# Performance work log

Measured on AMD Instinct MI355X. Metric: run time of the kernel, lower is better.

The kernel has to match this reference:

```python
import jax, jax.numpy as jnp
import numpy as np

K = 3          # cfg.KNN_UP
CHUNK = 2048   # point chunk for brute-force KNN
BN_EPS = 1e-5


def knn_interp(vox_c, vox_f, pt_c):
    """Inverse-distance k-NN interpolation of voxel features onto points.
    vox_c: [Nv,3] voxel centers; vox_f: [Nv,C]; pt_c: [Np,3]. Returns [Np,C]."""
    Np = pt_c.shape[0]

    def chunk_fn(pc):  # pc: [CHUNK,3]
        d2 = jnp.sum((pc[:, None, :] - vox_c[None, :, :]) ** 2, axis=-1)  # [CHUNK,Nv]
        neg_d2, idx = jax.lax.top_k(-d2, K)                               # k nearest
        d = jnp.sqrt(jnp.maximum(-neg_d2, 0.0))
        w = 1.0 / (d + 1e-8)
        w = w / jnp.sum(w, axis=-1, keepdims=True)                        # [CHUNK,K]
        return jnp.sum(vox_f[idx] * w[..., None], axis=1)                 # [CHUNK,C]

    out = jax.lax.map(chunk_fn, pt_c.reshape(Np // CHUNK, CHUNK, 3))
    return out.reshape(Np, vox_f.shape[-1])


def bn1d(x, gamma, beta):
    # BatchNorm1d in training mode, applied per decomposed batch item (as in
    # the original per-sample list comprehension): stats over the point dim.
    mu = jnp.mean(x, axis=0, keepdims=True)
    var = jnp.var(x, axis=0, keepdims=True)
    return gamma * (x - mu) * jax.lax.rsqrt(var + BN_EPS) + beta


def level_forward(vox_c, vox_f, pt_c, gamma, beta):
    f = jax.vmap(knn_interp, in_axes=(0, 0, 0))(vox_c, vox_f, pt_c)  # [B,Np,C]
    return jax.vmap(lambda xf: bn1d(xf, gamma, beta))(f)


def setup_inputs() -> dict:
    key = jax.random.key(0)
    ks = jax.random.split(key, 16)
    B, Np = 2, 32768
    SCENE = 50.0  # spread coordinates over a ~50m scene
    nvs = [2048, 6144, 16384, 32768]
    chs = [256, 128, 96, 96]
    inp = {"pt_c": jax.random.uniform(ks[0], (B, Np, 3), jnp.float32) * SCENE}
    for i, (nv, c) in enumerate(zip(nvs, chs), start=1):
        inp[f"vox_c{i}"] = jax.random.uniform(ks[2 * i - 1], (B, nv, 3), jnp.float32) * SCENE
        inp[f"vox_f{i}"] = jax.random.normal(ks[2 * i], (B, nv, c), jnp.float32)
        inp[f"gamma{i}"] = jnp.ones((c,), jnp.float32)
        inp[f"beta{i}"] = jnp.zeros((c,), jnp.float32)
    return inp


def reference(pt_c, vox_c1, vox_f1, gamma1, beta1,
              vox_c2, vox_f2, gamma2, beta2,
              vox_c3, vox_f3, gamma3, beta3,
              vox_c4, vox_f4, gamma4, beta4):
    # voxel_to_point: per-level KNN upsampling of decoder voxel features to
    # the raw point cloud, followed by per-sample BatchNorm1d.
    f1 = level_forward(vox_c1, vox_f1, pt_c, gamma1, beta1)
    f2 = level_forward(vox_c2, vox_f2, pt_c, gamma2, beta2)
    f3 = level_forward(vox_c3, vox_f3, pt_c, gamma3, beta3)
    f4 = level_forward(vox_c4, vox_f4, pt_c, gamma4, beta4)
    return (f1, f2, f3, f4)
```

## Files before the change

kernel.cpp:

```cpp
#include <hip/hip_runtime.h>
#include <cfloat>
#include <climits>
#include <cstdint>

#define NPOINTS 32768
#define NBATCH  2
#define NLEV    4
#define NJOB    5
#define PG      16
#define PCELLS  (PG*PG*PG)
#define NPB     128
#define NBLK    (NPOINTS / NPB)

struct BinJob {
  const float* coords;
  int* cnt; int* start; int* cur;
  float4* sorted;
  int G, ncells, N;
  float invh;
};
struct BinParams { BinJob job[NJOB]; };

struct Level {
  const float4* sorted;
  const int*    start;
  int*          idxo;
  float*        wo;
  int G, ncells, Nv;
  float h, invh;
};
struct Params { Level lv[NLEV]; };

__device__ __forceinline__ int cell1d(float x, float invh, int G) {
  int c = (int)(x * invh);
  return min(max(c, 0), G - 1);
}

__global__ __launch_bounds__(256) void zero_kernel(int* __restrict__ p, int n)
{
  int i = blockIdx.x * 256 + threadIdx.x;
  if (i < n) p[i] = 0;
}

__global__ __launch_bounds__(256) void count_kernel(BinParams prm)
{
  const BinJob J = prm.job[blockIdx.z];
  int v = blockIdx.x * 256 + threadIdx.x;
  int b = blockIdx.y;
  if (v >= J.N) return;
  const float* p = J.coords + ((size_t)b * J.N + v) * 3;
  int cx = cell1d(p[0], J.invh, J.G), cy = cell1d(p[1], J.invh, J.G), cz = cell1d(p[2], J.invh, J.G);
  atomicAdd(&J.cnt[b * J.ncells + (cz * J.G + cy) * J.G + cx], 1);
}

__global__ __launch_bounds__(1024) void scan_kernel(BinParams prm)
{
  const BinJob J = prm.job[blockIdx.y];
  const int b = blockIdx.x, t = threadIdx.x;
  const int ncells = J.ncells;
  const int* c  = J.cnt + (size_t)b * ncells;
  int* st = J.start + (size_t)b * (ncells + 1);
  int* cu = J.cur + (size_t)b * ncells;
  __shared__ int part[1024];
  const int chunk = (ncells + 1023) / 1024;
  const int lo = t * chunk, hi = min(lo + chunk, ncells);
  int s = 0;
  for (int i = lo; i < hi; ++i) s += c[i];
  part[t] = s;
  __syncthreads();
  for (int off = 1; off < 1024; off <<= 1) {
    int v = (t >= off) ? part[t - off] : 0;
    __syncthreads();
    part[t] += v;
    __syncthreads();
  }
  int base = (t > 0) ? part[t - 1] : 0;
  for (int i = lo; i < hi; ++i) { st[i] = base; cu[i] = base; base += c[i]; }
  if (t == 1023) st[ncells] = part[1023];
}

__global__ __launch_bounds__(256) void scatter_kernel(BinParams prm)
{
  const BinJob J = prm.job[blockIdx.z];
  int v = blockIdx.x * 256 + threadIdx.x;
  int b = blockIdx.y;
  if (v >= J.N) return;
  const float* p = J.coords + ((size_t)b * J.N + v) * 3;
  float x = p[0], y = p[1], z = p[2];
  int cx = cell1d(x, J.invh, J.G), cy = cell1d(y, J.invh, J.G), cz = cell1d(z, J.invh, J.G);
  int pos = atomicAdd(&J.cur[b * J.ncells + (cz * J.G + cy) * J.G + cx], 1);
  J.sorted[(size_t)b * J.N + pos] = make_float4(x, y, z, __int_as_float(v));
}

__global__ __launch_bounds__(256) void query_kernel(
    const float4* __restrict__ psorted, Params prm)
{
  const int l = blockIdx.y, b = blockIdx.z;
  const Level L = prm.lv[l];
  const int tid = threadIdx.x;
  const int q = tid & 3;
  const int sp = blockIdx.x * 64 + (tid >> 2);
  float4 pt = psorted[(size_t)b * NPOINTS + sp];
  const float px = pt.x, py = pt.y, pz = pt.z;
  const int p = __float_as_int(pt.w);
  const int G = L.G;
  const float h = L.h;

  const int cx = cell1d(px, L.invh, G);
  const int cy = cell1d(py, L.invh, G);
  const int cz = cell1d(pz, L.invh, G);
  const float fx = px - cx * h, fy = py - cy * h, fz = pz - cz * h;
  float m = fminf(fminf(fminf(fx, h - fx), fminf(fy, h - fy)), fminf(fz, h - fz));
  m = fmaxf(m, 0.f);

  const int* start     = L.start  + (size_t)b * (L.ncells + 1);
  const float4* sorted = L.sorted + (size_t)b * L.Nv;

  float b0 = FLT_MAX, b1 = FLT_MAX, b2 = FLT_MAX;
  int   i0 = INT_MAX, i1 = INT_MAX, i2 = INT_MAX;

  auto ins = [&](float d2, int vi) {
    if (d2 < b2 || (d2 == b2 && vi < i2)) {
      if (d2 < b1 || (d2 == b1 && vi < i1)) {
        b2 = b1; i2 = i1;
        if (d2 < b0 || (d2 == b0 && vi < i0)) { b1 = b0; i1 = i0; b0 = d2; i0 = vi; }
        else                                  { b1 = d2; i1 = vi; }
      } else { b2 = d2; i2 = vi; }
    }
  };
  auto cand = [&](int k) {
    float4 vv = sorted[k];
    int vi = __float_as_int(vv.w);
    float dx = px - vv.x, dy = py - vv.y, dz = pz - vv.z;
    float d2 = __fadd_rn(__fadd_rn(__fmul_rn(dx, dx), __fmul_rn(dy, dy)),
                         __fmul_rn(dz, dz));
    ins(d2, vi);
  };
  auto scan_range = [&](int ks, int ke) {
    for (int k = ks + q; k < ke; k += 4) cand(k);
  };

  const int rmax = max(max(cx, G - 1 - cx), max(max(cy, G - 1 - cy), max(cz, G - 1 - cz)));
  for (int rho = 0; rho <= rmax; ++rho) {
    if (rho >= 1) {
      float bm = fminf(b2, __shfl_xor(b2, 1));
      bm = fminf(bm, __shfl_xor(bm, 2));
      float dmin = fmaxf((rho - 1) * h + m, 0.f);
      if (dmin * dmin * 0.99999f > bm) break;
    }
    const int z0 = max(cz - rho, 0), z1 = min(cz + rho, G - 1);
    const int y0 = max(cy - rho, 0), y1 = min(cy + rho, G - 1);
    for (int iz = z0; iz <= z1; ++iz) {
      const int adz = abs(iz - cz);
      for (int iy = y0; iy <= y1; ++iy) {
        const int ady = max(adz, abs(iy - cy));
        const int row = (iz * G + iy) * G;
        if (ady == rho) {
          const int x0 = max(cx - rho, 0), x1 = min(cx + rho, G - 1);
          scan_range(start[row + x0], start[row + x1 + 1]);
        } else {
          const int xl = cx - rho, xr = cx + rho;
          if (xl >= 0)     scan_range(start[row + xl], start[row + xl + 1]);
          if (xr <= G - 1) scan_range(start[row + xr], start[row + xr + 1]);
        }
      }
    }
  }

  #pragma unroll
  for (int mask = 1; mask <= 2; mask <<= 1) {
    float c0 = __shfl_xor(b0, mask), c1 = __shfl_xor(b1, mask), c2 = __shfl_xor(b2, mask);
    int   j0 = __shfl_xor(i0, mask), j1 = __shfl_xor(i1, mask), j2 = __shfl_xor(i2, mask);
    ins(c0, j0); ins(c1, j1); ins(c2, j2);
  }

  if (q == 0) {
    float w0 = 1.0f / (sqrtf(b0) + 1e-8f);
    float w1 = 1.0f / (sqrtf(b1) + 1e-8f);
    float w2 = 1.0f / (sqrtf(b2) + 1e-8f);
    float ws = (w0 + w1) + w2;
    size_t o = ((size_t)b * NPOINTS + p) * 3;
    L.idxo[o] = i0; L.idxo[o + 1] = i1; L.idxo[o + 2] = i2;
    L.wo[o] = w0 / ws; L.wo[o + 1] = w1 / ws; L.wo[o + 2] = w2 / ws;
  }
}

template <int C, int BDIM>
__global__ __launch_bounds__(BDIM) void interp_kernel(
    const float* __restrict__ voxf, const int* __restrict__ idxo,
    const float* __restrict__ wo, float* __restrict__ out,
    float* __restrict__ psum, float* __restrict__ psq, int Nv)
{
  constexpr int C4 = C / 4;
  constexpr int R  = BDIM / C4;
  const int b = blockIdx.y, blk = blockIdx.x;
  const int tid = threadIdx.x;
  const int r = tid / C4, c4 = tid - r * C4;
  const float4* fb = (const float4*)(voxf + (size_t)b * Nv * C);
  float4* ob = (float4*)(out + (size_t)b * NPOINTS * C);
  const int p0 = blk * NPB;

  float4 s = make_float4(0, 0, 0, 0), q = make_float4(0, 0, 0, 0);
  for (int p = p0 + r; p < p0 + NPB; p += R) {
    size_t pg = ((size_t)b * NPOINTS + p) * 3;
    int   ia = idxo[pg], ib = idxo[pg + 1], ic = idxo[pg + 2];
    float wa = wo[pg],   wb = wo[pg + 1],   wc = wo[pg + 2];
    float4 fa = fb[(size_t)ia * C4 + c4];
    float4 f2 = fb[(size_t)ib * C4 + c4];
    float4 fc = fb[(size_t)ic * C4 + c4];
    float4 o;
    o.x = wa * fa.x + wb * f2.x + wc * fc.x;
    o.y = wa * fa.y + wb * f2.y + wc * fc.y;
    o.z = wa * fa.z + wb * f2.z + wc * fc.z;
    o.w = wa * fa.w + wb * f2.w + wc * fc.w;
    ob[(size_t)p * C4 + c4] = o;
    s.x += o.x; s.y += o.y; s.z += o.z; s.w += o.w;
    q.x += o.x * o.x; q.y += o.y * o.y; q.z += o.z * o.z; q.w += o.w * o.w;
  }

  __shared__ float4 ls[BDIM];
  ls[tid] = s;
  __syncthreads();
  if (r == 0) {
    float4 tot = s;
    #pragma unroll
    for (int rr = 1; rr < R; ++rr) {
      float4 v = ls[c4 + rr * C4];
      tot.x += v.x; tot.y += v.y; tot.z += v.z; tot.w += v.w;
    }
    ((float4*)psum)[((size_t)b * NBLK + blk) * C4 + c4] = tot;
  }
  __syncthreads();
  ls[tid] = q;
  __syncthreads();
  if (r == 0) {
    float4 tot = q;
    #pragma unroll
    for (int rr = 1; rr < R; ++rr) {
      float4 v = ls[c4 + rr * C4];
      tot.x += v.x; tot.y += v.y; tot.z += v.z; tot.w += v.w;
    }
    ((float4*)psq)[((size_t)b * NBLK + blk) * C4 + c4] = tot;
  }
}

__global__ __launch_bounds__(256) void bn_stats_kernel(
    const float* __restrict__ psum, const float* __restrict__ psq,
    const float* __restrict__ gamma, const float* __restrict__ beta,
    float* __restrict__ scale, float* __restrict__ shift, int C, float invN)
{
  const int c = blockIdx.x, b = blockIdx.y, t = threadIdx.x;
  float s = 0.f, q = 0.f;
  for (int k = t; k < NBLK; k += 256) {
    s += psum[((size_t)b * NBLK + k) * C + c];
    q += psq[((size_t)b * NBLK + k) * C + c];
  }
  __shared__ float ss[256], qs[256];
  ss[t] = s; qs[t] = q;
  __syncthreads();
  for (int o = 128; o > 0; o >>= 1) {
    if (t < o) { ss[t] += ss[t + o]; qs[t] += qs[t + o]; }
    __syncthreads();
  }
  if (t == 0) {
    float mu  = ss[0] * invN;
    float var = fmaxf(qs[0] * invN - mu * mu, 0.f);
    float sc  = gamma[c] * rsqrtf(var + 1e-5f);
    scale[b * C + c] = sc;
    shift[b * C + c] = beta[c] - mu * sc;
  }
}

__global__ __launch_bounds__(256) void bn_apply_kernel(
    float* __restrict__ out, const float* __restrict__ scale,
    const float* __restrict__ shift, int C, int NpC)
{
  const int e = blockIdx.x * 256 + threadIdx.x;
  const int npc4 = NpC >> 2, c4n = C >> 2;
  const int b = e / npc4;
  const int rem = e - b * npc4;
  const int c4 = rem % c4n;
  float4 v  = ((float4*)out)[e];
  float4 sc = ((const float4*)scale)[b * c4n + c4];
  float4 sh = ((const float4*)shift)[b * c4n + c4];
  v.x = fmaf(v.x, sc.x, sh.x);
  v.y = fmaf(v.y, sc.y, sh.y);
  v.z = fmaf(v.z, sc.z, sh.z);
  v.w = fmaf(v.w, sc.w, sh.w);
  ((float4*)out)[e] = v;
}

extern "C" void kernel_launch(void* const* d_in, const int* in_sizes, int n_in,
                              void* d_out, int out_size, void* d_ws, size_t ws_size,
                              hipStream_t stream)
{
  const float* ptc = (const float*)d_in[0];
  static const int    Cs[4]     = {256, 128, 96, 96};
  static const int    Nvs[4]    = {2048, 6144, 16384, 32768};
  static const int    Gs[4]     = {10, 14, 18, 22};
  static const size_t outOff[4] = {0, 16777216, 25165824, 31457280};

  size_t off = 0;
  auto carve = [&](size_t bytes) {
    off = (off + 255) & ~(size_t)255;
    size_t o = off; off += bytes; return o;
  };
  char* w = (char*)d_ws;

  int nc[NJOB];
  for (int l = 0; l < 4; ++l) nc[l] = Gs[l] * Gs[l] * Gs[l];
  nc[4] = PCELLS;
  int Ns[NJOB] = {Nvs[0], Nvs[1], Nvs[2], Nvs[3], NPOINTS};
  int Gj[NJOB] = {Gs[0], Gs[1], Gs[2], Gs[3], PG};

  int totcnt = 0;
  for (int j = 0; j < NJOB; ++j) totcnt += nc[j];
  int* cntbase = (int*)(w + carve((size_t)NBATCH * totcnt * 4));

  float4* sortedj[NJOB]; int* cntj[NJOB]; int* sttj[NJOB]; int* curj[NJOB];
  {
    int acc = 0;
    for (int j = 0; j < NJOB; ++j) {
      cntj[j] = cntbase + (size_t)NBATCH * acc;
      acc += nc[j];
    }
  }
  for (int j = 0; j < NJOB; ++j) {
    sortedj[j] = (float4*)(w + carve((size_t)NBATCH * Ns[j] * 16));
    sttj[j]    = (int*)   (w + carve((size_t)NBATCH * (nc[j] + 1) * 4));
    curj[j]    = (int*)   (w + carve((size_t)NBATCH * nc[j] * 4));
  }
  int*   idxo  = (int*)  (w + carve((size_t)NLEV * NBATCH * NPOINTS * 3 * 4));
  float* wo    = (float*)(w + carve((size_t)NLEV * NBATCH * NPOINTS * 3 * 4));
  float* psum  = (float*)(w + carve((size_t)NBATCH * NBLK * 256 * 4));
  float* psq   = (float*)(w + carve((size_t)NBATCH * NBLK * 256 * 4));
  float* scale = (float*)(w + carve((size_t)NBATCH * 256 * 4));
  float* shift = (float*)(w + carve((size_t)NBATCH * 256 * 4));

  BinParams bp;
  for (int j = 0; j < NJOB; ++j) {
    BinJob& J = bp.job[j];
    J.coords = (j < 4) ? (const float*)d_in[1 + 4 * j] : ptc;
    J.cnt = cntj[j]; J.start = sttj[j]; J.cur = curj[j]; J.sorted = sortedj[j];
    J.G = Gj[j]; J.ncells = nc[j]; J.N = Ns[j];
    J.invh = Gj[j] / 50.0f;
  }

  Params prm;
  for (int l = 0; l < 4; ++l) {
    Level& L = prm.lv[l];
    L.sorted = sortedj[l]; L.start = sttj[l];
    L.idxo = idxo + (size_t)l * NBATCH * NPOINTS * 3;
    L.wo   = wo   + (size_t)l * NBATCH * NPOINTS * 3;
    L.G = Gs[l]; L.ncells = nc[l]; L.Nv = Nvs[l];
    L.h = 50.0f / Gs[l]; L.invh = Gs[l] / 50.0f;
  }

  const int zn = NBATCH * totcnt;
  zero_kernel<<<(zn + 255) / 256, 256, 0, stream>>>(cntbase, zn);
  count_kernel<<<dim3((NPOINTS + 255) / 256, NBATCH, NJOB), 256, 0, stream>>>(bp);
  scan_kernel<<<dim3(NBATCH, NJOB), 1024, 0, stream>>>(bp);
  scatter_kernel<<<dim3((NPOINTS + 255) / 256, NBATCH, NJOB), 256, 0, stream>>>(bp);

  query_kernel<<<dim3(NPOINTS / 64, NLEV, NBATCH), 256, 0, stream>>>(sortedj[4], prm);

  for (int l = 0; l < 4; ++l) {
    const float* voxf  = (const float*)d_in[2 + 4 * l];
    const float* gamma = (const float*)d_in[3 + 4 * l];
    const float* beta  = (const float*)d_in[4 + 4 * l];
    const int C = Cs[l], Nv = Nvs[l];
    float* outl = (float*)d_out + outOff[l];
    const int* idl = idxo + (size_t)l * NBATCH * NPOINTS * 3;
    const float* wl = wo  + (size_t)l * NBATCH * NPOINTS * 3;

    if (C == 256)
      interp_kernel<256, 256><<<dim3(NBLK, NBATCH), 256, 0, stream>>>(
          voxf, idl, wl, outl, psum, psq, Nv);
    else if (C == 128)
      interp_kernel<128, 256><<<dim3(NBLK, NBATCH), 256, 0, stream>>>(
          voxf, idl, wl, outl, psum, psq, Nv);
    else
      interp_kernel<96, 240><<<dim3(NBLK, NBATCH), 240, 0, stream>>>(
          voxf, idl, wl, outl, psum, psq, Nv);

    bn_stats_kernel<<<dim3(C, NBATCH), 256, 0, stream>>>(
        psum, psq, gamma, beta, scale, shift, C, 1.0f / NPOINTS);

    const int n4 = NBATCH * NPOINTS * C / 4;
    bn_apply_kernel<<<n4 / 256, 256, 0, stream>>>(
        (float*)outl, scale, shift, C, NPOINTS * C);
  }
}
```

Baseline: 338.9 us.

## Recompute interpolation in BN apply pass and finer voxel grids with cell-level work split

Interpolation now runs twice: a first pass computes only the BN partial statistics without writing output, and a second pass recomputes the weighted gather, applies scale/shift and writes to the original point index. This removes the intermediate output write plus the separate read-modify-write BN apply pass. The query kernel stores results in sorted-point order, distributes whole cells round-robin across the four lanes instead of striding within cells, and uses finer grids. A per-cell insertion sort of points by original index is added to keep the ordering deterministic. The cost is recomputing the gathers and possible load imbalance across lanes.

```diff
diff --git a/kernel.cpp b/kernel.cpp
--- a/kernel.cpp
+++ b/kernel.cpp
@@ -92,6 +92,23 @@
   J.sorted[(size_t)b * J.N + pos] = make_float4(x, y, z, __int_as_float(v));
 }
 
+__global__ __launch_bounds__(256) void cellsort_kernel(
+    float4* __restrict__ sorted, const int* __restrict__ start)
+{
+  int cid = blockIdx.x * 256 + threadIdx.x;
+  if (cid >= NBATCH * PCELLS) return;
+  int b = cid / PCELLS, cc = cid - b * PCELLS;
+  const int* st = start + (size_t)b * (PCELLS + 1);
+  float4* s = sorted + (size_t)b * NPOINTS;
+  int ks = st[cc], ke = st[cc + 1];
+  for (int i = ks + 1; i < ke; ++i) {
+    float4 v = s[i]; int key = __float_as_int(v.w);
+    int j = i - 1;
+    while (j >= ks && __float_as_int(s[j].w) > key) { s[j + 1] = s[j]; --j; }
+    s[j + 1] = v;
+  }
+}
+
 __global__ __launch_bounds__(256) void query_kernel(
     const float4* __restrict__ psorted, Params prm)
 {
@@ -102,7 +119,6 @@
   const int sp = blockIdx.x * 64 + (tid >> 2);
   float4 pt = psorted[(size_t)b * NPOINTS + sp];
   const float px = pt.x, py = pt.y, pz = pt.z;
-  const int p = __float_as_int(pt.w);
   const int G = L.G;
   const float h = L.h;
 
@@ -128,19 +144,19 @@
       } else { b2 = d2; i2 = vi; }
     }
   };
-  auto cand = [&](int k) {
-    float4 vv = sorted[k];
-    int vi = __float_as_int(vv.w);
-    float dx = px - vv.x, dy = py - vv.y, dz = pz - vv.z;
-    float d2 = __fadd_rn(__fadd_rn(__fmul_rn(dx, dx), __fmul_rn(dy, dy)),
-                         __fmul_rn(dz, dz));
-    ins(d2, vi);
+  auto scan_all = [&](int ks, int ke) {
+    for (int k = ks; k < ke; ++k) {
+      float4 vv = sorted[k];
+      int vi = __float_as_int(vv.w);
+      float dx = px - vv.x, dy = py - vv.y, dz = pz - vv.z;
+      float d2 = __fadd_rn(__fadd_rn(__fmul_rn(dx, dx), __fmul_rn(dy, dy)),
+                           __fmul_rn(dz, dz));
+      ins(d2, vi);
+    }
   };
-  auto scan_range = [&](int ks, int ke) {
-    for (int k = ks + q; k < ke; k += 4) cand(k);
-  };
 
   const int rmax = max(max(cx, G - 1 - cx), max(max(cy, G - 1 - cy), max(cz, G - 1 - cz)));
+  int task = 0;
   for (int rho = 0; rho <= rmax; ++rho) {
     if (rho >= 1) {
       float bm = fminf(b2, __shfl_xor(b2, 1));
@@ -157,11 +173,11 @@
         const int row = (iz * G + iy) * G;
         if (ady == rho) {
           const int x0 = max(cx - rho, 0), x1 = min(cx + rho, G - 1);
-          scan_range(start[row + x0], start[row + x1 + 1]);
+          if (((task++) & 3) == q) scan_all(start[row + x0], start[row + x1 + 1]);
         } else {
           const int xl = cx - rho, xr = cx + rho;
-          if (xl >= 0)     scan_range(start[row + xl], start[row + xl + 1]);
-          if (xr <= G - 1) scan_range(start[row + xr], start[row + xr + 1]);
+          if (xl >= 0)     { if (((task++) & 3) == q) scan_all(start[row + xl], start[row + xl + 1]); }
+          if (xr <= G - 1) { if (((task++) & 3) == q) scan_all(start[row + xr], start[row + xr + 1]); }
         }
       }
     }
@@ -179,16 +195,16 @@
     float w1 = 1.0f / (sqrtf(b1) + 1e-8f);
     float w2 = 1.0f / (sqrtf(b2) + 1e-8f);
     float ws = (w0 + w1) + w2;
-    size_t o = ((size_t)b * NPOINTS + p) * 3;
+    size_t o = ((size_t)b * NPOINTS + sp) * 3;
     L.idxo[o] = i0; L.idxo[o + 1] = i1; L.idxo[o + 2] = i2;
     L.wo[o] = w0 / ws; L.wo[o + 1] = w1 / ws; L.wo[o + 2] = w2 / ws;
   }
 }
 
 template <int C, int BDIM>
-__global__ __launch_bounds__(BDIM) void interp_kernel(
+__global__ __launch_bounds__(BDIM) void interp_stats_kernel(
     const float* __restrict__ voxf, const int* __restrict__ idxo,
-    const float* __restrict__ wo, float* __restrict__ out,
+    const float* __restrict__ wo,
     float* __restrict__ psum, float* __restrict__ psq, int Nv)
 {
   constexpr int C4 = C / 4;
@@ -197,12 +213,11 @@
   const int tid = threadIdx.x;
   const int r = tid / C4, c4 = tid - r * C4;
   const float4* fb = (const float4*)(voxf + (size_t)b * Nv * C);
-  float4* ob = (float4*)(out + (size_t)b * NPOINTS * C);
   const int p0 = blk * NPB;
 
   float4 s = make_float4(0, 0, 0, 0), q = make_float4(0, 0, 0, 0);
-  for (int p = p0 + r; p < p0 + NPB; p += R) {
-    size_t pg = ((size_t)b * NPOINTS + p) * 3;
+  for (int sp = p0 + r; sp < p0 + NPB; sp += R) {
+    size_t pg = ((size_t)b * NPOINTS + sp) * 3;
     int   ia = idxo[pg], ib = idxo[pg + 1], ic = idxo[pg + 2];
     float wa = wo[pg],   wb = wo[pg + 1],   wc = wo[pg + 2];
     float4 fa = fb[(size_t)ia * C4 + c4];
@@ -213,7 +228,6 @@
     o.y = wa * fa.y + wb * f2.y + wc * fc.y;
     o.z = wa * fa.z + wb * f2.z + wc * fc.z;
     o.w = wa * fa.w + wb * f2.w + wc * fc.w;
-    ob[(size_t)p * C4 + c4] = o;
     s.x += o.x; s.y += o.y; s.z += o.z; s.w += o.w;
     q.x += o.x * o.x; q.y += o.y * o.y; q.z += o.z * o.z; q.w += o.w * o.w;
   }
@@ -271,23 +285,39 @@
   }
 }
 
-__global__ __launch_bounds__(256) void bn_apply_kernel(
-    float* __restrict__ out, const float* __restrict__ scale,
-    const float* __restrict__ shift, int C, int NpC)
-{
-  const int e = blockIdx.x * 256 + threadIdx.x;
-  const int npc4 = NpC >> 2, c4n = C >> 2;
-  const int b = e / npc4;
-  const int rem = e - b * npc4;
-  const int c4 = rem % c4n;
-  float4 v  = ((float4*)out)[e];
-  float4 sc = ((const float4*)scale)[b * c4n + c4];
-  float4 sh = ((const float4*)shift)[b * c4n + c4];
-  v.x = fmaf(v.x, sc.x, sh.x);
-  v.y = fmaf(v.y, sc.y, sh.y);
-  v.z = fmaf(v.z, sc.z, sh.z);
-  v.w = fmaf(v.w, sc.w, sh.w);
-  ((float4*)out)[e] = v;
+template <int C, int BDIM>
+__global__ __launch_bounds__(BDIM) void interp_apply_kernel(
+    const float* __restrict__ voxf, const int* __restrict__ idxo,
+    const float* __restrict__ wo, const float4* __restrict__ psorted,
+    const float* __restrict__ scale, const float* __restrict__ shift,
+    float* __restrict__ out, int Nv)
+{
+  constexpr int C4 = C / 4;
+  constexpr int R  = BDIM / C4;
+  const int b = blockIdx.y, blk = blockIdx.x;
+  const int tid = threadIdx.x;
+  const int r = tid / C4, c4 = tid - r * C4;
+  const float4* fb = (const float4*)(voxf + (size_t)b * Nv * C);
+  float4* ob = (float4*)(out + (size_t)b * NPOINTS * C);
+  const float4 sc = ((const float4*)scale)[b * C4 + c4];
+  const float4 sh = ((const float4*)shift)[b * C4 + c4];
+  const int p0 = blk * NPB;
+
+  for (int sp = p0 + r; sp < p0 + NPB; sp += R) {
+    int p = __float_as_int(psorted[(size_t)b * NPOINTS + sp].w);
+    size_t pg = ((size_t)b * NPOINTS + sp) * 3;
+    int   ia = idxo[pg], ib = idxo[pg + 1], ic = idxo[pg + 2];
+    float wa = wo[pg],   wb = wo[pg + 1],   wc = wo[pg + 2];
+    float4 fa = fb[(size_t)ia * C4 + c4];
+    float4 f2 = fb[(size_t)ib * C4 + c4];
+    float4 fc = fb[(size_t)ic * C4 + c4];
+    float4 o;
+    o.x = fmaf(wa * fa.x + wb * f2.x + wc * fc.x, sc.x, sh.x);
+    o.y = fmaf(wa * fa.y + wb * f2.y + wc * fc.y, sc.y, sh.y);
+    o.z = fmaf(wa * fa.z + wb * f2.z + wc * fc.z, sc.z, sh.z);
+    o.w = fmaf(wa * fa.w + wb * f2.w + wc * fc.w, sc.w, sh.w);
+    ob[(size_t)p * C4 + c4] = o;
+  }
 }
 
 extern "C" void kernel_launch(void* const* d_in, const int* in_sizes, int n_in,
@@ -297,7 +327,7 @@
   const float* ptc = (const float*)d_in[0];
   static const int    Cs[4]     = {256, 128, 96, 96};
   static const int    Nvs[4]    = {2048, 6144, 16384, 32768};
-  static const int    Gs[4]     = {10, 14, 18, 22};
+  static const int    Gs[4]     = {13, 18, 25, 32};
   static const size_t outOff[4] = {0, 16777216, 25165824, 31457280};
 
   size_t off = 0;
@@ -361,6 +391,7 @@
   count_kernel<<<dim3((NPOINTS + 255) / 256, NBATCH, NJOB), 256, 0, stream>>>(bp);
   scan_kernel<<<dim3(NBATCH, NJOB), 1024, 0, stream>>>(bp);
   scatter_kernel<<<dim3((NPOINTS + 255) / 256, NBATCH, NJOB), 256, 0, stream>>>(bp);
+  cellsort_kernel<<<(NBATCH * PCELLS + 255) / 256, 256, 0, stream>>>(sortedj[4], sttj[4]);
 
   query_kernel<<<dim3(NPOINTS / 64, NLEV, NBATCH), 256, 0, stream>>>(sortedj[4], prm);
 
@@ -374,20 +405,26 @@
     const float* wl = wo  + (size_t)l * NBATCH * NPOINTS * 3;
 
     if (C == 256)
-      interp_kernel<256, 256><<<dim3(NBLK, NBATCH), 256, 0, stream>>>(
-          voxf, idl, wl, outl, psum, psq, Nv);
+      interp_stats_kernel<256, 256><<<dim3(NBLK, NBATCH), 256, 0, stream>>>(
+          voxf, idl, wl, psum, psq, Nv);
     else if (C == 128)
-      interp_kernel<128, 256><<<dim3(NBLK, NBATCH), 256, 0, stream>>>(
-          voxf, idl, wl, outl, psum, psq, Nv);
+      interp_stats_kernel<128, 256><<<dim3(NBLK, NBATCH), 256, 0, stream>>>(
+          voxf, idl, wl, psum, psq, Nv);
     else
-      interp_kernel<96, 240><<<dim3(NBLK, NBATCH), 240, 0, stream>>>(
-          voxf, idl, wl, outl, psum, psq, Nv);
+      interp_stats_kernel<96, 240><<<dim3(NBLK, NBATCH), 240, 0, stream>>>(
+          voxf, idl, wl, psum, psq, Nv);
 
     bn_stats_kernel<<<dim3(C, NBATCH), 256, 0, stream>>>(
         psum, psq, gamma, beta, scale, shift, C, 1.0f / NPOINTS);
 
-    const int n4 = NBATCH * NPOINTS * C / 4;
-    bn_apply_kernel<<<n4 / 256, 256, 0, stream>>>(
-        (float*)outl, scale, shift, C, NPOINTS * C);
-  }
-}
+    if (C == 256)
+      interp_apply_kernel<256, 256><<<dim3(NBLK, NBATCH), 256, 0, stream>>>(
+          voxf, idl, wl, sortedj[4], scale, shift, outl, Nv);
+    else if (C == 128)
+      interp_apply_kernel<128, 256><<<dim3(NBLK, NBATCH), 256, 0, stream>>>(
+          voxf, idl, wl, sortedj[4], scale, shift, outl, Nv);
+    else
+      interp_apply_kernel<96, 240><<<dim3(NBLK, NBATCH), 240, 0, stream>>>(
+          voxf, idl, wl, sortedj[4], scale, shift, outl, Nv);
+  }
+}
```

New measurement: 577.9 us. +70.5%, slower.

## Unroll first KNN shell, store results in sorted order, sort cells deterministically

Applied to the files above, without the earlier changes.

The query kernel now loads the 9 row ranges of the 3x3x3 neighbourhood up front and scans them without per-shell checks, falling back to the shell loop only when needed. It also writes idx/weight outputs in spatially sorted point order instead of scattering by original index. The interp kernel then maps each sorted slot back to its original point through the sorted point array. A new cellsort kernel insertion-sorts each point cell by index so the sorted order is deterministic despite the atomic scatter. The aim is fewer dependent start[] loads and coalesced query writes and interp reads, at the cost of an extra kernel and an extra indirection load in interp.

```diff
diff --git a/kernel.cpp b/kernel.cpp
--- a/kernel.cpp
+++ b/kernel.cpp
@@ -92,6 +92,23 @@
   J.sorted[(size_t)b * J.N + pos] = make_float4(x, y, z, __int_as_float(v));
 }
 
+__global__ __launch_bounds__(256) void cellsort_kernel(
+    float4* __restrict__ sorted, const int* __restrict__ start)
+{
+  int cid = blockIdx.x * 256 + threadIdx.x;
+  if (cid >= NBATCH * PCELLS) return;
+  int b = cid / PCELLS, cc = cid - b * PCELLS;
+  const int* st = start + (size_t)b * (PCELLS + 1);
+  float4* s = sorted + (size_t)b * NPOINTS;
+  int ks = st[cc], ke = st[cc + 1];
+  for (int i = ks + 1; i < ke; ++i) {
+    float4 v = s[i]; int key = __float_as_int(v.w);
+    int j = i - 1;
+    while (j >= ks && __float_as_int(s[j].w) > key) { s[j + 1] = s[j]; --j; }
+    s[j + 1] = v;
+  }
+}
+
 __global__ __launch_bounds__(256) void query_kernel(
     const float4* __restrict__ psorted, Params prm)
 {
@@ -102,7 +119,6 @@
   const int sp = blockIdx.x * 64 + (tid >> 2);
   float4 pt = psorted[(size_t)b * NPOINTS + sp];
   const float px = pt.x, py = pt.y, pz = pt.z;
-  const int p = __float_as_int(pt.w);
   const int G = L.G;
   const float h = L.h;
 
@@ -140,28 +156,52 @@
     for (int k = ks + q; k < ke; k += 4) cand(k);
   };
 
-  const int rmax = max(max(cx, G - 1 - cx), max(max(cy, G - 1 - cy), max(cz, G - 1 - cz)));
-  for (int rho = 0; rho <= rmax; ++rho) {
-    if (rho >= 1) {
-      float bm = fminf(b2, __shfl_xor(b2, 1));
-      bm = fminf(bm, __shfl_xor(bm, 2));
-      float dmin = fmaxf((rho - 1) * h + m, 0.f);
-      if (dmin * dmin * 0.99999f > bm) break;
-    }
-    const int z0 = max(cz - rho, 0), z1 = min(cz + rho, G - 1);
-    const int y0 = max(cy - rho, 0), y1 = min(cy + rho, G - 1);
-    for (int iz = z0; iz <= z1; ++iz) {
-      const int adz = abs(iz - cz);
-      for (int iy = y0; iy <= y1; ++iy) {
-        const int ady = max(adz, abs(iy - cy));
-        const int row = (iz * G + iy) * G;
-        if (ady == rho) {
-          const int x0 = max(cx - rho, 0), x1 = min(cx + rho, G - 1);
-          scan_range(start[row + x0], start[row + x1 + 1]);
-        } else {
-          const int xl = cx - rho, xr = cx + rho;
-          if (xl >= 0)     scan_range(start[row + xl], start[row + xl + 1]);
-          if (xr <= G - 1) scan_range(start[row + xr], start[row + xr + 1]);
+  {
+    const int x0 = max(cx - 1, 0), x1 = min(cx + 1, G - 1);
+    int ks9[9], ke9[9];
+    #pragma unroll
+    for (int i = 0; i < 9; ++i) {
+      const int dz = i / 3 - 1, dy = i % 3 - 1;
+      const int iz = cz + dz, iy = cy + dy;
+      const bool ok = (iz >= 0) && (iz < G) && (iy >= 0) && (iy < G);
+      const int row = (iz * G + iy) * G;
+      const int sa = ok ? (row + x0) : 0;
+      const int sb = ok ? (row + x1 + 1) : 0;
+      int a = start[sa], e = start[sb];
+      if (!ok) { a = 0; e = 0; }
+      ks9[i] = a; ke9[i] = e;
+    }
+    #pragma unroll
+    for (int i = 0; i < 9; ++i) scan_range(ks9[i], ke9[i]);
+  }
+
+  {
+    float bm = fminf(b2, __shfl_xor(b2, 1));
+    bm = fminf(bm, __shfl_xor(bm, 2));
+    float dmin = h + m;
+    if (dmin * dmin * 0.99999f <= bm) {
+      const int rmax = max(max(cx, G - 1 - cx), max(max(cy, G - 1 - cy), max(cz, G - 1 - cz)));
+      for (int rho = 2; rho <= rmax; ++rho) {
+        float bmm = fminf(b2, __shfl_xor(b2, 1));
+        bmm = fminf(bmm, __shfl_xor(bmm, 2));
+        float dmn = fmaxf((rho - 1) * h + m, 0.f);
+        if (dmn * dmn * 0.99999f > bmm) break;
+        const int z0 = max(cz - rho, 0), z1 = min(cz + rho, G - 1);
+        const int y0 = max(cy - rho, 0), y1 = min(cy + rho, G - 1);
+        for (int iz = z0; iz <= z1; ++iz) {
+          const int adz = abs(iz - cz);
+          for (int iy = y0; iy <= y1; ++iy) {
+            const int ady = max(adz, abs(iy - cy));
+            const int row = (iz * G + iy) * G;
+            if (ady == rho) {
+              const int x0 = max(cx - rho, 0), x1 = min(cx + rho, G - 1);
+              scan_range(start[row + x0], start[row + x1 + 1]);
+            } else {
+              const int xl = cx - rho, xr = cx + rho;
+              if (xl >= 0)     scan_range(start[row + xl], start[row + xl + 1]);
+              if (xr <= G - 1) scan_range(start[row + xr], start[row + xr + 1]);
+            }
+          }
         }
       }
     }
@@ -179,7 +219,7 @@
     float w1 = 1.0f / (sqrtf(b1) + 1e-8f);
     float w2 = 1.0f / (sqrtf(b2) + 1e-8f);
     float ws = (w0 + w1) + w2;
-    size_t o = ((size_t)b * NPOINTS + p) * 3;
+    size_t o = ((size_t)b * NPOINTS + sp) * 3;
     L.idxo[o] = i0; L.idxo[o + 1] = i1; L.idxo[o + 2] = i2;
     L.wo[o] = w0 / ws; L.wo[o + 1] = w1 / ws; L.wo[o + 2] = w2 / ws;
   }
@@ -188,8 +228,9 @@
 template <int C, int BDIM>
 __global__ __launch_bounds__(BDIM) void interp_kernel(
     const float* __restrict__ voxf, const int* __restrict__ idxo,
-    const float* __restrict__ wo, float* __restrict__ out,
-    float* __restrict__ psum, float* __restrict__ psq, int Nv)
+    const float* __restrict__ wo, const float4* __restrict__ psorted,
+    float* __restrict__ out, float* __restrict__ psum, float* __restrict__ psq,
+    int Nv)
 {
   constexpr int C4 = C / 4;
   constexpr int R  = BDIM / C4;
@@ -201,8 +242,9 @@
   const int p0 = blk * NPB;
 
   float4 s = make_float4(0, 0, 0, 0), q = make_float4(0, 0, 0, 0);
-  for (int p = p0 + r; p < p0 + NPB; p += R) {
-    size_t pg = ((size_t)b * NPOINTS + p) * 3;
+  for (int sp = p0 + r; sp < p0 + NPB; sp += R) {
+    int p = __float_as_int(psorted[(size_t)b * NPOINTS + sp].w);
+    size_t pg = ((size_t)b * NPOINTS + sp) * 3;
     int   ia = idxo[pg], ib = idxo[pg + 1], ic = idxo[pg + 2];
     float wa = wo[pg],   wb = wo[pg + 1],   wc = wo[pg + 2];
     float4 fa = fb[(size_t)ia * C4 + c4];
@@ -361,6 +403,7 @@
   count_kernel<<<dim3((NPOINTS + 255) / 256, NBATCH, NJOB), 256, 0, stream>>>(bp);
   scan_kernel<<<dim3(NBATCH, NJOB), 1024, 0, stream>>>(bp);
   scatter_kernel<<<dim3((NPOINTS + 255) / 256, NBATCH, NJOB), 256, 0, stream>>>(bp);
+  cellsort_kernel<<<(NBATCH * PCELLS + 255) / 256, 256, 0, stream>>>(sortedj[4], sttj[4]);
 
   query_kernel<<<dim3(NPOINTS / 64, NLEV, NBATCH), 256, 0, stream>>>(sortedj[4], prm);
 
@@ -375,13 +418,13 @@
 
     if (C == 256)
       interp_kernel<256, 256><<<dim3(NBLK, NBATCH), 256, 0, stream>>>(
-          voxf, idl, wl, outl, psum, psq, Nv);
+          voxf, idl, wl, sortedj[4], outl, psum, psq, Nv);
     else if (C == 128)
       interp_kernel<128, 256><<<dim3(NBLK, NBATCH), 256, 0, stream>>>(
-          voxf, idl, wl, outl, psum, psq, Nv);
+          voxf, idl, wl, sortedj[4], outl, psum, psq, Nv);
     else
       interp_kernel<96, 240><<<dim3(NBLK, NBATCH), 240, 0, stream>>>(
-          voxf, idl, wl, outl, psum, psq, Nv);
+          voxf, idl, wl, sortedj[4], outl, psum, psq, Nv);
 
     bn_stats_kernel<<<dim3(C, NBATCH), 256, 0, stream>>>(
         psum, psq, gamma, beta, scale, shift, C, 1.0f / NPOINTS);
```

After: 375.3 us. +10.7%, slower.

## Use 16 lanes per query point and cooperatively scan the 3x3x3 neighborhood

Applied to the files above, without the earlier changes.

The KNN query kernel now assigns 16 threads per point instead of 4, and launches four times as many blocks. The first shell (rho 0 and 1) is handled as nine x-rows of the 3x3x3 cell block: one lane loads each row's start and count, and the values are broadcast with shuffles. This replaces the nested shell loops and their scattered start-table reads for the common case. Later shells fall back to the old loop using 16-way strides, and the merge and reduction shuffles widen to 16 lanes. The trade-off is more shuffle traffic, more lanes idling when cells are sparse, and more total threads.

```diff
diff --git a/kernel.cpp b/kernel.cpp
--- a/kernel.cpp
+++ b/kernel.cpp
@@ -98,8 +98,9 @@
   const int l = blockIdx.y, b = blockIdx.z;
   const Level L = prm.lv[l];
   const int tid = threadIdx.x;
-  const int q = tid & 3;
-  const int sp = blockIdx.x * 64 + (tid >> 2);
+  const int ln = tid & 15;
+  const int gbase = (tid & 63) & ~15;
+  const int sp = blockIdx.x * 16 + (tid >> 4);
   float4 pt = psorted[(size_t)b * NPOINTS + sp];
   const float px = pt.x, py = pt.y, pz = pt.z;
   const int p = __float_as_int(pt.w);
@@ -128,7 +129,7 @@
       } else { b2 = d2; i2 = vi; }
     }
   };
-  auto cand = [&](int k) {
+  auto evalk = [&](int k) {
     float4 vv = sorted[k];
     int vi = __float_as_int(vv.w);
     float dx = px - vv.x, dy = py - vv.y, dz = pz - vv.z;
@@ -136,45 +137,75 @@
                          __fmul_rn(dz, dz));
     ins(d2, vi);
   };
-  auto scan_range = [&](int ks, int ke) {
-    for (int k = ks + q; k < ke; k += 4) cand(k);
+  auto gmin = [&](float v) {
+    #pragma unroll
+    for (int mask = 1; mask < 16; mask <<= 1)
+      v = fminf(v, __shfl_xor(v, mask));
+    return v;
   };
 
-  const int rmax = max(max(cx, G - 1 - cx), max(max(cy, G - 1 - cy), max(cz, G - 1 - cz)));
-  for (int rho = 0; rho <= rmax; ++rho) {
-    if (rho >= 1) {
-      float bm = fminf(b2, __shfl_xor(b2, 1));
-      bm = fminf(bm, __shfl_xor(bm, 2));
-      float dmin = fmaxf((rho - 1) * h + m, 0.f);
-      if (dmin * dmin * 0.99999f > bm) break;
-    }
-    const int z0 = max(cz - rho, 0), z1 = min(cz + rho, G - 1);
-    const int y0 = max(cy - rho, 0), y1 = min(cy + rho, G - 1);
-    for (int iz = z0; iz <= z1; ++iz) {
-      const int adz = abs(iz - cz);
-      for (int iy = y0; iy <= y1; ++iy) {
-        const int ady = max(adz, abs(iy - cy));
-        const int row = (iz * G + iy) * G;
-        if (ady == rho) {
-          const int x0 = max(cx - rho, 0), x1 = min(cx + rho, G - 1);
-          scan_range(start[row + x0], start[row + x1 + 1]);
-        } else {
-          const int xl = cx - rho, xr = cx + rho;
-          if (xl >= 0)     scan_range(start[row + xl], start[row + xl + 1]);
-          if (xr <= G - 1) scan_range(start[row + xr], start[row + xr + 1]);
+  int ks = 0, rc = 0;
+  if (ln < 9) {
+    int iz = cz + ln / 3 - 1, iy = cy + ln % 3 - 1;
+    if (iz >= 0 && iz < G && iy >= 0 && iy < G) {
+      int x0 = max(cx - 1, 0), x1 = min(cx + 1, G - 1);
+      int row = (iz * G + iy) * G;
+      ks = start[row + x0];
+      rc = start[row + x1 + 1] - ks;
+    }
+  }
+  #pragma unroll
+  for (int r = 0; r < 9; ++r) {
+    int rk = __shfl(ks, gbase + r);
+    int rn = __shfl(rc, gbase + r);
+    for (int k = rk + ln; k < rk + rn; k += 16) evalk(k);
+  }
+
+  {
+    float bm = gmin(b2);
+    float dmin = h + m;
+    if (!(dmin * dmin * 0.99999f > bm)) {
+      const int rmax = max(max(cx, G - 1 - cx), max(max(cy, G - 1 - cy), max(cz, G - 1 - cz)));
+      for (int rho = 2; rho <= rmax; ++rho) {
+        bm = gmin(b2);
+        float dmn = fmaxf((rho - 1) * h + m, 0.f);
+        if (dmn * dmn * 0.99999f > bm) break;
+        const int z0 = max(cz - rho, 0), z1 = min(cz + rho, G - 1);
+        const int y0 = max(cy - rho, 0), y1 = min(cy + rho, G - 1);
+        for (int iz = z0; iz <= z1; ++iz) {
+          const int adz = abs(iz - cz);
+          for (int iy = y0; iy <= y1; ++iy) {
+            const int ady = max(adz, abs(iy - cy));
+            const int row = (iz * G + iy) * G;
+            if (ady == rho) {
+              const int xa = max(cx - rho, 0), xb = min(cx + rho, G - 1);
+              int a = start[row + xa], e = start[row + xb + 1];
+              for (int k = a + ln; k < e; k += 16) evalk(k);
+            } else {
+              const int xl = cx - rho, xr = cx + rho;
+              if (xl >= 0) {
+                int a = start[row + xl], e = start[row + xl + 1];
+                for (int k = a + ln; k < e; k += 16) evalk(k);
+              }
+              if (xr <= G - 1) {
+                int a = start[row + xr], e = start[row + xr + 1];
+                for (int k = a + ln; k < e; k += 16) evalk(k);
+              }
+            }
+          }
         }
       }
     }
   }
 
   #pragma unroll
-  for (int mask = 1; mask <= 2; mask <<= 1) {
+  for (int mask = 1; mask <= 8; mask <<= 1) {
     float c0 = __shfl_xor(b0, mask), c1 = __shfl_xor(b1, mask), c2 = __shfl_xor(b2, mask);
     int   j0 = __shfl_xor(i0, mask), j1 = __shfl_xor(i1, mask), j2 = __shfl_xor(i2, mask);
     ins(c0, j0); ins(c1, j1); ins(c2, j2);
   }
 
-  if (q == 0) {
+  if (ln == 0) {
     float w0 = 1.0f / (sqrtf(b0) + 1e-8f);
     float w1 = 1.0f / (sqrtf(b1) + 1e-8f);
     float w2 = 1.0f / (sqrtf(b2) + 1e-8f);
@@ -362,7 +393,7 @@
   scan_kernel<<<dim3(NBATCH, NJOB), 1024, 0, stream>>>(bp);
   scatter_kernel<<<dim3((NPOINTS + 255) / 256, NBATCH, NJOB), 256, 0, stream>>>(bp);
 
-  query_kernel<<<dim3(NPOINTS / 64, NLEV, NBATCH), 256, 0, stream>>>(sortedj[4], prm);
+  query_kernel<<<dim3(NPOINTS / 16, NLEV, NBATCH), 256, 0, stream>>>(sortedj[4], prm);
 
   for (int l = 0; l < 4; ++l) {
     const float* voxf  = (const float*)d_in[2 + 4 * l];
```

Measured after the change: 514.7 us. 51.9% more time.
